# Optimization experiments

Hardware: AMD Instinct MI355X
Metric: run time of the kernel (lower is better)

The kernel has to match this reference:

```python
import jax, jax.numpy as jnp
import numpy as np

K = 6                 # color-coding parameter; K-1 message-passing steps
N = 50000             # num nodes
E = 1600000           # num edges (avg degree 32)
F = 384               # num_node_features = K * 2**K


def setup_inputs() -> dict:
    key = jax.random.key(0)
    k1, k2, k3, k4, k5 = jax.random.split(key, 5)
    s = 1.0 / np.sqrt(F)
    x = jax.random.normal(k1, (N, F), dtype=jnp.float32)
    edge_index = jax.random.randint(k2, (2, E), 0, N, dtype=jnp.int32)
    batch = jnp.zeros((N,), dtype=jnp.int32)  # unused by forward, kept for signature parity
    W_rel = jax.random.normal(k3, (F, F), dtype=jnp.float32) * s   # GraphConv lin_rel weight
    W_root = jax.random.normal(k4, (F, F), dtype=jnp.float32) * s  # GraphConv lin_root weight
    W_lin = jax.random.normal(k5, (1, F), dtype=jnp.float32) * s   # readout linear (no bias)
    return {"x": x, "edge_index": edge_index, "batch": batch,
            "W_rel": W_rel, "W_root": W_root, "W_lin": W_lin}


def reference(x, edge_index, batch, W_rel, W_root, W_lin):
    src = edge_index[0]
    dst = edge_index[1]
    # K-1 iterations of PyG GraphConv(aggr='add', bias=False) + relu:
    #   out = segment_sum(x[src] -> dst) @ W_rel^T + x @ W_root^T
    for _ in range(K - 1):
        agg = jax.ops.segment_sum(x[src], dst, num_segments=N)  # [N, F]
        x = jax.nn.relu(agg @ W_rel.T + x @ W_root.T)
    # readout: Linear(F, 1, bias=False)
    return x @ W_lin.T  # [N, 1]
```

## Files before the change

### kernel.cpp

```cpp
#include <hip/hip_runtime.h>
#include <hip/hip_bf16.h>

#define NN 50000
#define EE 1600000
#define FF 384
#define MPAD 50048
#define NITER 5

typedef unsigned int u32;
typedef unsigned short u16;
typedef __attribute__((ext_vector_type(8))) short short8;
typedef __attribute__((ext_vector_type(4))) float f32x4;

typedef const __attribute__((address_space(1))) void* gptr_t;
typedef __attribute__((address_space(3))) void* lptr_t;

__device__ __forceinline__ float bf_lo(u32 u) {
  u32 v = u << 16;
  return __builtin_bit_cast(float, v);
}
__device__ __forceinline__ float bf_hi(u32 u) {
  u32 v = u & 0xFFFF0000u;
  return __builtin_bit_cast(float, v);
}
__device__ __forceinline__ u32 f2bf(float f) {
  u32 u = __builtin_bit_cast(u32, f);
  return (u + 0x7FFFu + ((u >> 16) & 1u)) >> 16;
}
__device__ __forceinline__ u32 pack2(float lo, float hi) {
  return f2bf(lo) | (f2bf(hi) << 16);
}
__device__ __forceinline__ void load16_lds(const void* g, void* l) {
  __builtin_amdgcn_global_load_lds((gptr_t)g, (lptr_t)l, 16, 0, 0);
}

__global__ void hist_kernel(const int* __restrict__ key, int* __restrict__ cnt) {
  int e = blockIdx.x * 256 + threadIdx.x;
  if (e < EE) atomicAdd(&cnt[key[e]], 1);
}

__global__ void scan_kernel(const int* __restrict__ cnt, int* __restrict__ row_start,
                            int* __restrict__ cursor) {
  __shared__ int wsum[4];
  const int CH = 196;
  int t = threadIdx.x;
  int lo = t * CH;
  int hi = lo + CH; if (hi > NN) hi = NN;
  int s = 0;
  int n4 = (hi - lo) >> 2;
  const int4* p = (const int4*)(cnt + lo);
  for (int i = 0; i < n4; ++i) { int4 c = p[i]; s += c.x + c.y + c.z + c.w; }
  int lane = t & 63, w = t >> 6;
  int v = s;
  for (int d = 1; d < 64; d <<= 1) { int u = __shfl_up(v, d, 64); if (lane >= d) v += u; }
  if (lane == 63) wsum[w] = v;
  __syncthreads();
  int run = v - s;
  for (int i = 0; i < w; ++i) run += wsum[i];
  int4* q1 = (int4*)(row_start + lo);
  int4* q2 = (int4*)(cursor + lo);
  for (int k = 0; k < n4; ++k) {
    int4 c = p[k];
    int4 o; o.x = run; o.y = run + c.x; o.z = o.y + c.y; o.w = o.z + c.z;
    run = o.w + c.w;
    q1[k] = o; q2[k] = o;
  }
  if (hi == NN && lo < NN) row_start[NN] = run;
}

__global__ void scatter_kernel(const int* __restrict__ src, const int* __restrict__ dst,
                               int* __restrict__ cursor, int* __restrict__ col) {
  int e = blockIdx.x * 256 + threadIdx.x;
  if (e < EE) {
    int d = dst[e];
    int p = atomicAdd(&cursor[d], 1);
    col[p] = src[e];
  }
}

__global__ void convert_x_kernel(const float* __restrict__ xin, u16* __restrict__ xout) {
  size_t i = ((size_t)blockIdx.x * 256 + threadIdx.x) * 4;
  if (i >= (size_t)NN * FF) return;
  float4 f = *(const float4*)(xin + i);
  u32 o0 = pack2(f.x, f.y);
  u32 o1 = pack2(f.z, f.w);
  u32* q = (u32*)(xout + i);
  q[0] = o0; q[1] = o1;
}

__global__ void build_bt_kernel(const float* __restrict__ Wr, const float* __restrict__ Wt,
                                u16* __restrict__ Bt) {
  int i = blockIdx.x * 256 + threadIdx.x;
  if (i >= FF * 2 * FF) return;
  int n = i / (2 * FF);
  int k = i - n * (2 * FF);
  float v = (k < FF) ? Wr[n * FF + k] : Wt[n * FF + (k - FF)];
  Bt[i] = (u16)f2bf(v);
}

__global__ void spmm_kernel(const u16* __restrict__ x, const int* __restrict__ rs,
                            const int* __restrict__ col, u16* __restrict__ agg) {
  int row = blockIdx.x * 4 + (threadIdx.x >> 6);
  int lane = threadIdx.x & 63;
  if (row >= NN) return;
  int j0 = rs[row], j1 = rs[row + 1];
  float a0 = 0.f, a1 = 0.f, a2 = 0.f, a3 = 0.f, a4 = 0.f, a5 = 0.f;
  int j = j0;
  for (; j + 2 <= j1; j += 2) {
    int s0 = col[j], s1 = col[j + 1];
    const u32* p0 = (const u32*)(x + (size_t)s0 * FF) + lane * 3;
    const u32* p1 = (const u32*)(x + (size_t)s1 * FF) + lane * 3;
    u32 u0 = p0[0], u1 = p0[1], u2 = p0[2];
    u32 v0 = p1[0], v1 = p1[1], v2 = p1[2];
    a0 += bf_lo(u0); a1 += bf_hi(u0);
    a2 += bf_lo(u1); a3 += bf_hi(u1);
    a4 += bf_lo(u2); a5 += bf_hi(u2);
    a0 += bf_lo(v0); a1 += bf_hi(v0);
    a2 += bf_lo(v1); a3 += bf_hi(v1);
    a4 += bf_lo(v2); a5 += bf_hi(v2);
  }
  if (j < j1) {
    int s0 = col[j];
    const u32* p0 = (const u32*)(x + (size_t)s0 * FF) + lane * 3;
    u32 u0 = p0[0], u1 = p0[1], u2 = p0[2];
    a0 += bf_lo(u0); a1 += bf_hi(u0);
    a2 += bf_lo(u1); a3 += bf_hi(u1);
    a4 += bf_lo(u2); a5 += bf_hi(u2);
  }
  u32* q = (u32*)(agg + (size_t)row * FF) + lane * 3;
  q[0] = pack2(a0, a1);
  q[1] = pack2(a2, a3);
  q[2] = pack2(a4, a5);
}

__global__ __launch_bounds__(512, 4) void gemm_kernel(
    const u16* __restrict__ Aagg, const u16* __restrict__ Ax,
    const u16* __restrict__ Bt, u16* __restrict__ Xout) {
  __shared__ __align__(16) u16 As[2][64 * 64];
  __shared__ __align__(16) u16 Bs[384 * 64];

  const int orig = blockIdx.x;
  const int xcd = orig & 7, idx = orig >> 3;
  const int wg = ((xcd < 6) ? xcd * 98 : 6 * 98 + (xcd - 6) * 97) + idx;
  const int m0 = wg * 64;

  const int tid = threadIdx.x;
  const int lane = tid & 63;
  const int w = tid >> 6;
  const int wr = w >> 2;
  const int wc = w & 3;

  f32x4 acc[2][6] = {};

#define STAGE_A(KT, BUF)                                                        \
  {                                                                             \
    const u16* Asrc_ = ((KT) < 6) ? Aagg : Ax;                                  \
    const int kbA_ = (((KT) < 6) ? (KT) : (KT)-6) << 7;                         \
    const int rA_ = tid >> 3;                                                   \
    const int bcA_ = (tid & 7) << 4;                                            \
    load16_lds((const char*)Asrc_ + (size_t)(m0 + rA_) * 768 + kbA_ +           \
                   (bcA_ ^ ((rA_ & 7) << 4)),                                   \
               (char*)&As[BUF][0] + tid * 16);                                  \
  }

#define STAGE_B(KT)                                                             \
  {                                                                             \
    const int kbB_ = (KT) << 7;                                                 \
    _Pragma("unroll")                                                           \
    for (int i = 0; i < 6; ++i) {                                               \
      const int c = tid + i * 512;                                              \
      const int rB_ = c >> 3;                                                   \
      const int bcB_ = (c & 7) << 4;                                            \
      load16_lds((const char*)Bt + (size_t)rB_ * 1536 + kbB_ +                  \
                     (bcB_ ^ ((rB_ & 7) << 4)),                                 \
                 (char*)&Bs[0] + c * 16);                                       \
    }                                                                           \
  }

  STAGE_A(0, 0);
  STAGE_B(0);
  __syncthreads();

  int buf = 0;
  for (int kt = 0; kt < 12; ++kt) {
    if (kt < 11) STAGE_A(kt + 1, buf ^ 1);
#pragma unroll
    for (int ks = 0; ks < 2; ++ks) {
      short8 af[2], bfm[6];
#pragma unroll
      for (int ni = 0; ni < 6; ++ni) {
        const int r = wc * 96 + ni * 16 + (lane & 15);
        const int bc = (ks * 64 + ((lane >> 4) << 4)) ^ ((r & 7) << 4);
        bfm[ni] = *(const short8*)((const char*)&Bs[0] + r * 128 + bc);
      }
#pragma unroll
      for (int mi = 0; mi < 2; ++mi) {
        const int r = wr * 32 + mi * 16 + (lane & 15);
        const int bc = (ks * 64 + ((lane >> 4) << 4)) ^ ((r & 7) << 4);
        af[mi] = *(const short8*)((const char*)&As[buf][0] + r * 128 + bc);
      }
#pragma unroll
      for (int mi = 0; mi < 2; ++mi)
#pragma unroll
        for (int ni = 0; ni < 6; ++ni)
          acc[mi][ni] = __builtin_amdgcn_mfma_f32_16x16x32_bf16(af[mi], bfm[ni], acc[mi][ni], 0, 0, 0);
    }
    __syncthreads();
    if (kt < 11) {
      STAGE_B(kt + 1);
      __syncthreads();
    }
    buf ^= 1;
  }

#pragma unroll
  for (int mi = 0; mi < 2; ++mi) {
#pragma unroll
    for (int r = 0; r < 4; ++r) {
      const int row = m0 + wr * 32 + mi * 16 + ((lane >> 4) << 2) + r;
      u16* orow = Xout + (size_t)row * FF + wc * 96 + (lane & 15);
#pragma unroll
      for (int ni = 0; ni < 6; ++ni) {
        float v = fmaxf(acc[mi][ni][r], 0.0f);
        orow[ni * 16] = (u16)f2bf(v);
      }
    }
  }
#undef STAGE_A
#undef STAGE_B
}

__global__ void readout_kernel(const u16* __restrict__ x, const float* __restrict__ wl,
                               float* __restrict__ out) {
  int row = blockIdx.x * 4 + (threadIdx.x >> 6);
  int lane = threadIdx.x & 63;
  if (row >= NN) return;
  const u32* p = (const u32*)(x + (size_t)row * FF) + lane * 3;
  u32 u0 = p[0], u1 = p[1], u2 = p[2];
  const float* w = wl + lane * 6;
  float s = bf_lo(u0) * w[0] + bf_hi(u0) * w[1] +
            bf_lo(u1) * w[2] + bf_hi(u1) * w[3] +
            bf_lo(u2) * w[4] + bf_hi(u2) * w[5];
#pragma unroll
  for (int off = 32; off > 0; off >>= 1) s += __shfl_down(s, off, 64);
  if (lane == 0) out[row] = s;
}

extern "C" void kernel_launch(void* const* d_in, const int* in_sizes, int n_in,
                              void* d_out, int out_size, void* d_ws, size_t ws_size,
                              hipStream_t stream) {
  const float* x_in = (const float*)d_in[0];
  const int* ei = (const int*)d_in[1];
  const float* W_rel = (const float*)d_in[3];
  const float* W_root = (const float*)d_in[4];
  const float* W_lin = (const float*)d_in[5];
  float* out = (float*)d_out;

  char* ws = (char*)d_ws;
  int* cnt = (int*)(ws);
  int* row_start = (int*)(ws + 200064);
  int* cursor = (int*)(ws + 400128);
  int* col = (int*)(ws + 600192);
  u16* Bt = (u16*)(ws + 7000192);
  u16* agg = (u16*)(ws + 7590016);
  u16* x0 = (u16*)(ws + 46026880);
  u16* x1 = (u16*)(ws + 84463744);
  if (ws_size < (size_t)122900608) return;

  const int* esrc = ei;
  const int* edst = ei + EE;

  hipMemsetAsync(cnt, 0, NN * sizeof(int), stream);
  hipMemsetAsync(agg + (size_t)NN * FF, 0, (size_t)(MPAD - NN) * FF * sizeof(u16), stream);
  hipMemsetAsync(x0 + (size_t)NN * FF, 0, (size_t)(MPAD - NN) * FF * sizeof(u16), stream);
  hipMemsetAsync(x1 + (size_t)NN * FF, 0, (size_t)(MPAD - NN) * FF * sizeof(u16), stream);

  hist_kernel<<<EE / 256, 256, 0, stream>>>(edst, cnt);
  scan_kernel<<<1, 256, 0, stream>>>(cnt, row_start, cursor);
  scatter_kernel<<<EE / 256, 256, 0, stream>>>(esrc, edst, cursor, col);
  convert_x_kernel<<<(NN * FF / 4 + 255) / 256, 256, 0, stream>>>(x_in, x0);
  build_bt_kernel<<<(FF * 2 * FF + 255) / 256, 256, 0, stream>>>(W_rel, W_root, Bt);

  u16* xs = x0;
  u16* xd = x1;
  for (int t = 0; t < NITER; ++t) {
    spmm_kernel<<<NN / 4, 256, 0, stream>>>(xs, row_start, col, agg);
    gemm_kernel<<<MPAD / 64, 512, 0, stream>>>(agg, xs, Bt, xd);
    u16* tmp = xs; xs = xd; xd = tmp;
  }
  readout_kernel<<<NN / 4, 256, 0, stream>>>(xs, W_lin, out);
}
```

Before: 1.278 ms.

## Split SpMM gather into three feature-slice passes with 8-way unrolled loads

The neighbour aggregation is split into three launches, each covering a 128-feature slice (64 u32 words per row). Each wave lane then loads one u32 per neighbour instead of three, and the edge loop is unrolled by eight so more independent gathers are in flight. The slicing is meant to shrink the working set per pass (50000 rows × 256 B) so gathered rows stay in L2/MALL cache. In exchange the CSR index array is read three times, each 256-byte row segment gives less coalescing per gather, and every iteration launches two more kernels.

```diff
diff --git a/kernel.cpp b/kernel.cpp
--- a/kernel.cpp
+++ b/kernel.cpp
@@ -98,39 +98,37 @@
   Bt[i] = (u16)f2bf(v);
 }
 
-__global__ void spmm_kernel(const u16* __restrict__ x, const int* __restrict__ rs,
-                            const int* __restrict__ col, u16* __restrict__ agg) {
+__global__ void spmm_pass_kernel(const u16* __restrict__ x, const int* __restrict__ rs,
+                                 const int* __restrict__ col, u16* __restrict__ agg,
+                                 const int fo) {
   int row = blockIdx.x * 4 + (threadIdx.x >> 6);
   int lane = threadIdx.x & 63;
   if (row >= NN) return;
   int j0 = rs[row], j1 = rs[row + 1];
-  float a0 = 0.f, a1 = 0.f, a2 = 0.f, a3 = 0.f, a4 = 0.f, a5 = 0.f;
+  float alo = 0.f, ahi = 0.f;
+  const u32* xw = (const u32*)x + fo + lane;
   int j = j0;
-  for (; j + 2 <= j1; j += 2) {
-    int s0 = col[j], s1 = col[j + 1];
-    const u32* p0 = (const u32*)(x + (size_t)s0 * FF) + lane * 3;
-    const u32* p1 = (const u32*)(x + (size_t)s1 * FF) + lane * 3;
-    u32 u0 = p0[0], u1 = p0[1], u2 = p0[2];
-    u32 v0 = p1[0], v1 = p1[1], v2 = p1[2];
-    a0 += bf_lo(u0); a1 += bf_hi(u0);
-    a2 += bf_lo(u1); a3 += bf_hi(u1);
-    a4 += bf_lo(u2); a5 += bf_hi(u2);
-    a0 += bf_lo(v0); a1 += bf_hi(v0);
-    a2 += bf_lo(v1); a3 += bf_hi(v1);
-    a4 += bf_lo(v2); a5 += bf_hi(v2);
-  }
-  if (j < j1) {
-    int s0 = col[j];
-    const u32* p0 = (const u32*)(x + (size_t)s0 * FF) + lane * 3;
-    u32 u0 = p0[0], u1 = p0[1], u2 = p0[2];
-    a0 += bf_lo(u0); a1 += bf_hi(u0);
-    a2 += bf_lo(u1); a3 += bf_hi(u1);
-    a4 += bf_lo(u2); a5 += bf_hi(u2);
-  }
-  u32* q = (u32*)(agg + (size_t)row * FF) + lane * 3;
-  q[0] = pack2(a0, a1);
-  q[1] = pack2(a2, a3);
-  q[2] = pack2(a4, a5);
+  for (; j + 8 <= j1; j += 8) {
+    int s0 = col[j + 0], s1 = col[j + 1], s2 = col[j + 2], s3 = col[j + 3];
+    int s4 = col[j + 4], s5 = col[j + 5], s6 = col[j + 6], s7 = col[j + 7];
+    u32 u0 = xw[(size_t)s0 * 192];
+    u32 u1 = xw[(size_t)s1 * 192];
+    u32 u2 = xw[(size_t)s2 * 192];
+    u32 u3 = xw[(size_t)s3 * 192];
+    u32 u4 = xw[(size_t)s4 * 192];
+    u32 u5 = xw[(size_t)s5 * 192];
+    u32 u6 = xw[(size_t)s6 * 192];
+    u32 u7 = xw[(size_t)s7 * 192];
+    alo += bf_lo(u0) + bf_lo(u1) + bf_lo(u2) + bf_lo(u3) +
+           bf_lo(u4) + bf_lo(u5) + bf_lo(u6) + bf_lo(u7);
+    ahi += bf_hi(u0) + bf_hi(u1) + bf_hi(u2) + bf_hi(u3) +
+           bf_hi(u4) + bf_hi(u5) + bf_hi(u6) + bf_hi(u7);
+  }
+  for (; j < j1; ++j) {
+    u32 u = xw[(size_t)col[j] * 192];
+    alo += bf_lo(u); ahi += bf_hi(u);
+  }
+  ((u32*)agg)[(size_t)row * 192 + fo + lane] = pack2(alo, ahi);
 }
 
 __global__ __launch_bounds__(512, 4) void gemm_kernel(
@@ -284,7 +282,8 @@
   u16* xs = x0;
   u16* xd = x1;
   for (int t = 0; t < NITER; ++t) {
-    spmm_kernel<<<NN / 4, 256, 0, stream>>>(xs, row_start, col, agg);
+    for (int p = 0; p < 3; ++p)
+      spmm_pass_kernel<<<NN / 4, 256, 0, stream>>>(xs, row_start, col, agg, p * 64);
     gemm_kernel<<<MPAD / 64, 512, 0, stream>>>(agg, xs, Bt, xd);
     u16* tmp = xs; xs = xd; xd = tmp;
   }
```

Result: no change. 1.265 ms (-1.0%).
